# Kernel tuning notes

Measured on AMD Instinct MI355X. Metric: run time of the kernel, lower is better.

The kernel has to match this reference:

```python
import jax, jax.numpy as jnp
import numpy as np

N_ATOMS = 100_000
N_BONDS = 200_000
MAX_NB = 6
ATOM_FDIM = 133
BOND_FDIM = 147
HIDDEN = 256
DEPTH = 5
ATOMS_PER_MOL = 100


def setup_inputs() -> dict:
    key = jax.random.key(0)
    ks = jax.random.split(key, 9)
    f_atoms = jax.random.normal(ks[0], (N_ATOMS, ATOM_FDIM), dtype=jnp.float32)
    f_bonds = jax.random.normal(ks[1], (N_BONDS, BOND_FDIM), dtype=jnp.float32)
    a2b = jax.random.randint(ks[2], (N_ATOMS, MAX_NB), 0, N_BONDS, dtype=jnp.int32)
    b2a = jax.random.randint(ks[3], (N_BONDS,), 0, N_ATOMS, dtype=jnp.int32)
    # reverse bond of 2i is 2i+1 and vice versa (chemprop directed-bond pairing)
    b2revb = (jnp.arange(N_BONDS, dtype=jnp.int32) ^ 1)
    s_i = 1.0 / np.sqrt(BOND_FDIM)
    s_h = 1.0 / np.sqrt(HIDDEN)
    s_o = 1.0 / np.sqrt(ATOM_FDIM + HIDDEN)
    W_i = jax.random.uniform(ks[4], (HIDDEN, BOND_FDIM), jnp.float32, -s_i, s_i)
    W_h = jax.random.uniform(ks[5], (HIDDEN, HIDDEN), jnp.float32, -s_h, s_h)
    W_o = jax.random.uniform(ks[6], (HIDDEN, ATOM_FDIM + HIDDEN), jnp.float32, -s_o, s_o)
    b_o = jax.random.uniform(ks[7], (HIDDEN,), jnp.float32, -s_o, s_o)
    return {"f_atoms": f_atoms, "f_bonds": f_bonds, "a2b": a2b, "b2a": b2a,
            "b2revb": b2revb, "W_i": W_i, "W_h": W_h, "W_o": W_o, "b_o": b_o,
            "atoms_per_mol": ATOMS_PER_MOL}


def reference(f_atoms, f_bonds, a2b, b2a, b2revb, W_i, W_h, W_o, b_o, atoms_per_mol):
    # input = W_i(f_bonds); message = relu(input)   [n_bonds, H]
    inp = jnp.einsum('bf,hf->bh', f_bonds, W_i)
    message = jax.nn.relu(inp)
    for _ in range(DEPTH - 1):
        # gather incoming-bond messages per atom and sum: [n_atoms, max_nb, H] -> [n_atoms, H]
        a_message = message[a2b].sum(axis=1)
        # directed-MPNN update: subtract reverse-bond message
        m = a_message[b2a] - message[b2revb]
        message = jax.nn.relu(inp + jnp.einsum('bh,gh->bg', m, W_h))
        # dropout p=0.0 (eval) -> identity
    a_message = message[a2b].sum(axis=1)                      # [n_atoms, H]
    a_input = jnp.concatenate([f_atoms, a_message], axis=1)   # [n_atoms, atom_fdim+H]
    atom_hiddens = jax.nn.relu(jnp.einsum('af,hf->ah', a_input, W_o) + b_o)
    # uniform a_scope: stack per-molecule atom blocks -> [n_mols, atoms_per_mol, H]
    return atom_hiddens.reshape(-1, atoms_per_mol, HIDDEN)
```

## Files before the change

### kernel.cpp

```cpp
#include <hip/hip_runtime.h>
#include <hip/hip_bf16.h>

typedef unsigned short u16;
typedef unsigned short u16x8 __attribute__((ext_vector_type(8)));
typedef short s8vec __attribute__((ext_vector_type(8)));
typedef float f4vec __attribute__((ext_vector_type(4)));

__device__ __forceinline__ float bf2f(u16 u) {
    union { unsigned int i; float f; } c; c.i = ((unsigned int)u) << 16; return c.f;
}
__device__ __forceinline__ u16 f2bfc(float f) {
    __hip_bfloat16 h = __float2bfloat16(f);
    return __builtin_bit_cast(u16, h);
}
__device__ __forceinline__ void gload_lds16(const void* g, void* l) {
    __builtin_amdgcn_global_load_lds((__attribute__((address_space(1))) void*)g,
                                     (__attribute__((address_space(3))) void*)l, 16, 0, 0);
}

__global__ void pad_rows(const float* __restrict__ src, u16* __restrict__ dst,
                         int rows, int scol, int dcol) {
    size_t total4 = (size_t)rows * dcol / 4;
    for (size_t i = blockIdx.x * (size_t)blockDim.x + threadIdx.x; i < total4;
         i += (size_t)gridDim.x * blockDim.x) {
        size_t idx = i * 4;
        int r = (int)(idx / dcol);
        int c = (int)(idx % dcol);
        const float* s = src + (size_t)r * scol + c;
        ushort4 o;
        o.x = (c + 0 < scol) ? f2bfc(s[0]) : (u16)0;
        o.y = (c + 1 < scol) ? f2bfc(s[1]) : (u16)0;
        o.z = (c + 2 < scol) ? f2bfc(s[2]) : (u16)0;
        o.w = (c + 3 < scol) ? f2bfc(s[3]) : (u16)0;
        *(ushort4*)(dst + idx) = o;
    }
}

__global__ void pad_w_all(const float* __restrict__ W_i, const float* __restrict__ W_h,
                          const float* __restrict__ W_o,
                          u16* __restrict__ Wi, u16* __restrict__ Wh,
                          u16* __restrict__ Wo2, u16* __restrict__ Wo1) {
    int r = blockIdx.x;
    int which = blockIdx.y;
    const float* src; u16* dst; int sstride, col0, nvalid, dcol;
    if (which == 0)      { src = W_i; dst = Wi;  sstride = 147; col0 = 0;   nvalid = 147; dcol = 192; }
    else if (which == 1) { src = W_h; dst = Wh;  sstride = 256; col0 = 0;   nvalid = 256; dcol = 256; }
    else if (which == 2) { src = W_o; dst = Wo2; sstride = 389; col0 = 133; nvalid = 256; dcol = 256; }
    else                 { src = W_o; dst = Wo1; sstride = 389; col0 = 0;   nvalid = 133; dcol = 192; }
    for (int c = threadIdx.x; c < dcol; c += blockDim.x) {
        float v = (c < nvalid) ? src[(size_t)r * sstride + col0 + c] : 0.f;
        dst[(size_t)r * dcol + c] = f2bfc(v);
    }
}

__global__ void gather6_kernel(const u16* __restrict__ P, const int* __restrict__ a2b,
                               u16* __restrict__ out, int n_atoms) {
    int lane = threadIdx.x & 63;
    int half = lane >> 5;
    int col = (lane & 31) * 8;
    int wid = (blockIdx.x * blockDim.x + threadIdx.x) >> 6;
    int nw = (gridDim.x * blockDim.x) >> 6;
    for (int a0 = wid * 2; a0 < n_atoms; a0 += nw * 2) {
        int a = a0 + half;
        const int* idx = a2b + a * 6;
        int2 i01 = *(const int2*)idx;
        int2 i23 = *(const int2*)(idx + 2);
        int2 i45 = *(const int2*)(idx + 4);
        u16x8 v0 = *(const u16x8*)(P + (size_t)i01.x * 256 + col);
        u16x8 v1 = *(const u16x8*)(P + (size_t)i01.y * 256 + col);
        u16x8 v2 = *(const u16x8*)(P + (size_t)i23.x * 256 + col);
        u16x8 v3 = *(const u16x8*)(P + (size_t)i23.y * 256 + col);
        u16x8 v4 = *(const u16x8*)(P + (size_t)i45.x * 256 + col);
        u16x8 v5 = *(const u16x8*)(P + (size_t)i45.y * 256 + col);
        u16x8 o;
#pragma unroll
        for (int e = 0; e < 8; ++e)
            o[e] = f2bfc(((bf2f(v0[e]) + bf2f(v1[e])) + (bf2f(v2[e]) + bf2f(v3[e])))
                         + (bf2f(v4[e]) + bf2f(v5[e])));
        *(u16x8*)(out + (size_t)a * 256 + col) = o;
    }
}

template <int ASTAGE, int EPI, int KP>
__launch_bounds__(1024, 4)
__global__ void gemm_smem(const u16* __restrict__ Asrc, const u16* __restrict__ Pm,
                          const u16* __restrict__ aPm, const int* __restrict__ b2a,
                          const u16* __restrict__ Bw, int M,
                          void* __restrict__ out0, const u16* __restrict__ aQ,
                          const float* __restrict__ bias) {
    constexpr int CPR = KP / 8;
    constexpr int NKS = KP / 32;
    __shared__ __align__(16) char smem[256 * KP * 2];

    const int t = threadIdx.x;
    const int w = t >> 6, lane = t & 63;
    const int ln15 = lane & 15, hi = lane >> 4;

    constexpr int ITER = (256 * CPR) / 1024;
#pragma unroll
    for (int i = 0; i < ITER; ++i) {
        int d = i * 1024 + t;
        int row = d / CPR, pc = d % CPR;
        int c = pc ^ (row & 7);
        gload_lds16(Bw + (size_t)row * KP + c * 8, &smem[(size_t)(i * 1024 + w * 64) * 16]);
    }
    __syncthreads();

    const int ntiles = M / 16;
    const int cnt = (ntiles + gridDim.x - 1) / gridDim.x;
    const int tile0 = blockIdx.x * cnt;

    for (int it = w; it < cnt; it += 16) {
        const int tile = tile0 + it;
        if (tile >= ntiles) break;
        const int r0 = tile * 16;
        const int gr = r0 + ln15;
        const u16* pi = Asrc + (size_t)gr * KP;
        const u16* pp = nullptr; const u16* pv = nullptr;
        if (ASTAGE == 4) {
            pp = Pm + (size_t)(gr ^ 1) * KP;
            pv = aPm + (size_t)b2a[gr] * KP;
        }

        u16x8 a[NKS];
#pragma unroll
        for (int ks = 0; ks < NKS; ++ks) {
            const int co = ks * 32 + hi * 8;
            if (ASTAGE == 0) {
                a[ks] = *(const u16x8*)(pi + co);
            } else if (ASTAGE == 2) {
                u16x8 vi = *(const u16x8*)(pi + co);
                u16x8 v;
#pragma unroll
                for (int e = 0; e < 8; ++e) v[e] = (vi[e] >> 15) ? (u16)0 : vi[e];
                a[ks] = v;
            } else {
                u16x8 vi = __builtin_nontemporal_load((const u16x8*)(pi + co));
                u16x8 vp = *(const u16x8*)(pp + co);
                u16x8 va = *(const u16x8*)(pv + co);
                u16x8 v;
#pragma unroll
                for (int e = 0; e < 8; ++e)
                    v[e] = f2bfc(fmaxf(bf2f(vi[e]) + bf2f(va[e]) - bf2f(vp[e]), 0.f));
                a[ks] = v;
            }
        }

        f4vec acc[16];
#pragma unroll
        for (int j = 0; j < 16; ++j) acc[j] = (f4vec){0.f, 0.f, 0.f, 0.f};
        __builtin_amdgcn_s_setprio(1);
#pragma unroll
        for (int ks = 0; ks < NKS; ++ks) {
#pragma unroll
            for (int j = 0; j < 16; ++j) {
                const int rowc = j * 16 + ln15;
                const int phys = (ks * 4 + hi) ^ (rowc & 7);
                s8vec bf = *(const s8vec*)&smem[rowc * (CPR * 16) + phys * 16];
                acc[j] = __builtin_amdgcn_mfma_f32_16x16x32_bf16(
                    *(const s8vec*)&a[ks], bf, acc[j], 0, 0, 0);
            }
        }
        __builtin_amdgcn_s_setprio(0);

#pragma unroll
        for (int j = 0; j < 16; ++j) {
            const int C = j * 16 + ln15;
#pragma unroll
            for (int r = 0; r < 4; ++r) {
                const int R = r0 + hi * 4 + r;
                float vv = acc[j][r];
                if (EPI == 0) {
                    ((u16*)out0)[(size_t)R * 256 + C] = f2bfc(vv);
                } else {
                    float o = vv + bf2f(aQ[(size_t)R * 256 + C]) + bias[C];
                    ((float*)out0)[(size_t)R * 256 + C] = fmaxf(o, 0.f);
                }
            }
        }
    }
}

extern "C" void kernel_launch(void* const* d_in, const int* in_sizes, int n_in,
                              void* d_out, int out_size, void* d_ws, size_t ws_size,
                              hipStream_t stream) {
    const float* f_atoms = (const float*)d_in[0];
    const float* f_bonds = (const float*)d_in[1];
    const int* a2b = (const int*)d_in[2];
    const int* b2a = (const int*)d_in[3];
    const float* W_i = (const float*)d_in[5];
    const float* W_h = (const float*)d_in[6];
    const float* W_o = (const float*)d_in[7];
    const float* b_o = (const float*)d_in[8];

    const int NA = 100000, NB = 200000;

    char* ws = (char*)d_ws;
    u16* fb  = (u16*)(ws + 0);
    u16* fa  = (u16*)(ws + 0);
    u16* inp = (u16*)(ws + 76800000);
    u16* Pa  = (u16*)(ws + 179200000);
    u16* Pb  = (u16*)(ws + 281600000);
    u16* aP  = (u16*)(ws + 384000000);
    u16* Wi  = (u16*)(ws + 435200000);
    u16* Wh  = (u16*)(ws + 435298304);
    u16* Wo2 = (u16*)(ws + 435429376);
    u16* Wo1 = (u16*)(ws + 435560448);
    if (ws_size < 435658752u) return;

    pad_w_all<<<dim3(256, 4), dim3(256), 0, stream>>>(W_i, W_h, W_o, Wi, Wh, Wo2, Wo1);
    pad_rows<<<dim3(2048), dim3(256), 0, stream>>>(f_bonds, fb, NB, 147, 192);

    gemm_smem<0, 0, 192><<<dim3(256), dim3(1024), 0, stream>>>(
        fb, nullptr, nullptr, nullptr, Wi, NB, inp, nullptr, nullptr);

    gemm_smem<2, 0, 256><<<dim3(256), dim3(1024), 0, stream>>>(
        inp, nullptr, nullptr, nullptr, Wh, NB, Pa, nullptr, nullptr);
    gather6_kernel<<<dim3(2048), dim3(256), 0, stream>>>(Pa, a2b, aP, NA);

    u16* Pcur = Pa; u16* Pnxt = Pb;
    for (int it = 0; it < 3; ++it) {
        gemm_smem<4, 0, 256><<<dim3(256), dim3(1024), 0, stream>>>(
            inp, Pcur, aP, b2a, Wh, NB, Pnxt, nullptr, nullptr);
        gather6_kernel<<<dim3(2048), dim3(256), 0, stream>>>(Pnxt, a2b, aP, NA);
        u16* tmp = Pcur; Pcur = Pnxt; Pnxt = tmp;
    }

    gemm_smem<4, 0, 256><<<dim3(256), dim3(1024), 0, stream>>>(
        inp, Pcur, aP, b2a, Wo2, NB, Pnxt, nullptr, nullptr);
    gather6_kernel<<<dim3(2048), dim3(256), 0, stream>>>(Pnxt, a2b, aP, NA);

    pad_rows<<<dim3(2048), dim3(256), 0, stream>>>(f_atoms, fa, NA, 133, 192);

    gemm_smem<0, 3, 192><<<dim3(256), dim3(1024), 0, stream>>>(
        fa, nullptr, nullptr, nullptr, Wo1, NA, d_out, aP, b_o);
}
```

Before: 921.1 us.

## Fuse neighbor gather-sum into message GEMM A-operand load

Replaces the separate per-atom gather6 kernel inside the depth loop with an in-GEMM gather: each bond row loads its atom's six incoming-bond messages directly from P and sums them in fp32 before the reverse-bond subtraction and ReLU. This removes the aP intermediate write/read and several kernel launches. It roughly doubles the random gather reads, since each atom's neighbors are now re-read per bond instead of once per atom. It also drops the nontemporal hint on the inp load.

```diff
diff --git a/kernel.cpp b/kernel.cpp
--- a/kernel.cpp
+++ b/kernel.cpp
@@ -84,7 +84,7 @@
 template <int ASTAGE, int EPI, int KP>
 __launch_bounds__(1024, 4)
 __global__ void gemm_smem(const u16* __restrict__ Asrc, const u16* __restrict__ Pm,
-                          const u16* __restrict__ aPm, const int* __restrict__ b2a,
+                          const int* __restrict__ a2b_g, const int* __restrict__ b2a,
                           const u16* __restrict__ Bw, int M,
                           void* __restrict__ out0, const u16* __restrict__ aQ,
                           const float* __restrict__ bias) {
@@ -116,10 +116,19 @@
         const int r0 = tile * 16;
         const int gr = r0 + ln15;
         const u16* pi = Asrc + (size_t)gr * KP;
-        const u16* pp = nullptr; const u16* pv = nullptr;
-        if (ASTAGE == 4) {
+        const u16* pp = nullptr;
+        const u16 *n0 = nullptr, *n1 = nullptr, *n2 = nullptr,
+                  *n3 = nullptr, *n4 = nullptr, *n5 = nullptr;
+        if (ASTAGE == 5) {
             pp = Pm + (size_t)(gr ^ 1) * KP;
-            pv = aPm + (size_t)b2a[gr] * KP;
+            int atom = b2a[gr];
+            const int* nidx = a2b_g + (size_t)atom * 6;
+            int2 j01 = *(const int2*)nidx;
+            int2 j23 = *(const int2*)(nidx + 2);
+            int2 j45 = *(const int2*)(nidx + 4);
+            n0 = Pm + (size_t)j01.x * KP;  n1 = Pm + (size_t)j01.y * KP;
+            n2 = Pm + (size_t)j23.x * KP;  n3 = Pm + (size_t)j23.y * KP;
+            n4 = Pm + (size_t)j45.x * KP;  n5 = Pm + (size_t)j45.y * KP;
         }
 
         u16x8 a[NKS];
@@ -135,13 +144,25 @@
                 for (int e = 0; e < 8; ++e) v[e] = (vi[e] >> 15) ? (u16)0 : vi[e];
                 a[ks] = v;
             } else {
-                u16x8 vi = __builtin_nontemporal_load((const u16x8*)(pi + co));
+                u16x8 vi = *(const u16x8*)(pi + co);
                 u16x8 vp = *(const u16x8*)(pp + co);
-                u16x8 va = *(const u16x8*)(pv + co);
+                u16x8 x0 = *(const u16x8*)(n0 + co);
+                u16x8 x1 = *(const u16x8*)(n1 + co);
+                float s[8];
+#pragma unroll
+                for (int e = 0; e < 8; ++e) s[e] = bf2f(x0[e]) + bf2f(x1[e]);
+                x0 = *(const u16x8*)(n2 + co);
+                x1 = *(const u16x8*)(n3 + co);
+#pragma unroll
+                for (int e = 0; e < 8; ++e) s[e] += bf2f(x0[e]) + bf2f(x1[e]);
+                x0 = *(const u16x8*)(n4 + co);
+                x1 = *(const u16x8*)(n5 + co);
+#pragma unroll
+                for (int e = 0; e < 8; ++e) s[e] += bf2f(x0[e]) + bf2f(x1[e]);
                 u16x8 v;
 #pragma unroll
                 for (int e = 0; e < 8; ++e)
-                    v[e] = f2bfc(fmaxf(bf2f(vi[e]) + bf2f(va[e]) - bf2f(vp[e]), 0.f));
+                    v[e] = f2bfc(fmaxf(bf2f(vi[e]) + s[e] - bf2f(vp[e]), 0.f));
                 a[ks] = v;
             }
         }
@@ -201,7 +222,7 @@
     u16* inp = (u16*)(ws + 76800000);
     u16* Pa  = (u16*)(ws + 179200000);
     u16* Pb  = (u16*)(ws + 281600000);
-    u16* aP  = (u16*)(ws + 384000000);
+    u16* aQ  = (u16*)(ws + 384000000);
     u16* Wi  = (u16*)(ws + 435200000);
     u16* Wh  = (u16*)(ws + 435298304);
     u16* Wo2 = (u16*)(ws + 435429376);
@@ -216,22 +237,20 @@
 
     gemm_smem<2, 0, 256><<<dim3(256), dim3(1024), 0, stream>>>(
         inp, nullptr, nullptr, nullptr, Wh, NB, Pa, nullptr, nullptr);
-    gather6_kernel<<<dim3(2048), dim3(256), 0, stream>>>(Pa, a2b, aP, NA);
 
     u16* Pcur = Pa; u16* Pnxt = Pb;
     for (int it = 0; it < 3; ++it) {
-        gemm_smem<4, 0, 256><<<dim3(256), dim3(1024), 0, stream>>>(
-            inp, Pcur, aP, b2a, Wh, NB, Pnxt, nullptr, nullptr);
-        gather6_kernel<<<dim3(2048), dim3(256), 0, stream>>>(Pnxt, a2b, aP, NA);
+        gemm_smem<5, 0, 256><<<dim3(256), dim3(1024), 0, stream>>>(
+            inp, Pcur, a2b, b2a, Wh, NB, Pnxt, nullptr, nullptr);
         u16* tmp = Pcur; Pcur = Pnxt; Pnxt = tmp;
     }
 
-    gemm_smem<4, 0, 256><<<dim3(256), dim3(1024), 0, stream>>>(
-        inp, Pcur, aP, b2a, Wo2, NB, Pnxt, nullptr, nullptr);
-    gather6_kernel<<<dim3(2048), dim3(256), 0, stream>>>(Pnxt, a2b, aP, NA);
+    gemm_smem<5, 0, 256><<<dim3(256), dim3(1024), 0, stream>>>(
+        inp, Pcur, a2b, b2a, Wo2, NB, Pnxt, nullptr, nullptr);
+    gather6_kernel<<<dim3(2048), dim3(256), 0, stream>>>(Pnxt, a2b, aQ, NA);
 
     pad_rows<<<dim3(2048), dim3(256), 0, stream>>>(f_atoms, fa, NA, 133, 192);
 
     gemm_smem<0, 3, 192><<<dim3(256), dim3(1024), 0, stream>>>(
-        fa, nullptr, nullptr, nullptr, Wo1, NA, d_out, aP, b_o);
-}
+        fa, nullptr, nullptr, nullptr, Wo1, NA, d_out, aQ, b_o);
+}
```

After: 1.285 ms. 1.39x slower.
